# Kernel tuning notes

Hardware: AMD Instinct MI355X
Metric: run time of the kernel (lower is better)

## Reference

```python
import jax, jax.numpy as jnp
import numpy as np

R_MAX = 5.0          # MACE default cutoff
P_CUT = 6            # polynomial cutoff exponent
AVG_NEIGH = 16.0     # MACE avg_num_neighbors normalization


def _sph_harm(u):
    """Real spherical harmonics l=0..3, e3nn 'component' normalization. u: [E,3] unit vectors -> [E,16]."""
    x, y, z = u[..., 0], u[..., 1], u[..., 2]
    s3, s5, s15 = np.sqrt(3.0), np.sqrt(5.0), np.sqrt(15.0)
    s35_8, s105, s21_8, s7 = np.sqrt(35.0 / 8.0), np.sqrt(105.0), np.sqrt(21.0 / 8.0), np.sqrt(7.0)
    one = jnp.ones_like(x)
    Y = [
        one,
        s3 * x, s3 * y, s3 * z,
        s15 * x * y, s15 * y * z, 0.5 * s5 * (3.0 * z * z - 1.0), s15 * x * z, 0.5 * s15 * (x * x - y * y),
        s35_8 * y * (3.0 * x * x - y * y), s105 * x * y * z, s21_8 * y * (5.0 * z * z - 1.0),
        0.5 * s7 * (5.0 * z * z * z - 3.0 * z), s21_8 * x * (5.0 * z * z - 1.0),
        0.5 * s105 * z * (x * x - y * y), s35_8 * x * (x * x - 3.0 * y * y),
    ]
    return jnp.stack(Y, axis=-1)


def _radial_embedding(r):
    """Bessel basis (8) times polynomial cutoff. r: [E] -> [E,8]."""
    n = jnp.arange(1, 9, dtype=r.dtype)
    rb = np.sqrt(2.0 / R_MAX) * jnp.sin(n * jnp.pi * r[:, None] / R_MAX) / r[:, None]
    uu = jnp.clip(r / R_MAX, 0.0, 1.0)
    p = float(P_CUT)
    f = (1.0 - 0.5 * (p + 1.0) * (p + 2.0) * uu ** p
         + p * (p + 2.0) * uu ** (p + 1.0)
         - 0.5 * p * (p + 1.0) * uu ** (p + 2.0))
    return rb * f[:, None]


def _forward(positions, shifts, node_attrs, W_embed, W_up, W_r1, W_r2, W_lin, W_skip, W_prod, Wcg, Wcg2, edge_index):
    N = positions.shape[0]
    snd, rcv = edge_index[0], edge_index[1]
    vec = positions[rcv] - positions[snd] + shifts            # [E,3]
    r = jnp.sqrt(jnp.maximum(jnp.sum(vec * vec, -1), 1e-12))  # [E]
    u = vec / r[:, None]
    edge_attrs = _sph_harm(u)                                 # [E,16]
    edge_feats = _radial_embedding(r)                         # [E,8]
    L = edge_attrs.shape[-1]
    k = W_embed.shape[1]
    # node embedding: scalars in the l=0 slot
    feats = jnp.zeros((N, k, L), positions.dtype).at[:, :, 0].set(node_attrs @ W_embed)
    invariants = []
    for i in range(W_up.shape[0]):
        up = jnp.einsum('nkL,kc->ncL', feats, W_up[i])                      # linear_up
        Rw = jax.nn.silu(edge_feats @ W_r1[i]) @ W_r2[i]                    # radial MLP [E,k]
        gathered = up[snd] * Rw[:, :, None]                                 # [E,k,16]
        # equivariant tensor product (coupling tensor plays the CG role)
        msg = jnp.einsum('eka,es,ast->ekt', gathered, edge_attrs, Wcg)      # [E,k,16]
        agg = jax.ops.segment_sum(msg, rcv, num_segments=N) / AVG_NEIGH     # scatter-sum
        mid = jnp.einsum('nkL,kc->ncL', agg, W_lin[i])
        # residual skip tensor product with species attrs
        sc = jnp.einsum('nkL,nz,zkc->ncL', feats, node_attrs, W_skip[i])
        # product block: symmetric (quadratic) contraction + linear + skip
        quad = jnp.einsum('nka,nkb,abt->nkt', mid, mid, Wcg2)
        feats = jnp.einsum('nkL,kc->ncL', mid + quad, W_prod[i]) + sc
        invariants.append(feats[:, :, 0])                                   # l=0 invariant slice [N,k]
    return jnp.concatenate(invariants, axis=-1)                             # [N, n_layers*k]


def setup_inputs() -> dict:
    key = jax.random.key(0)
    ks = jax.random.split(key, 12)
    N, E, Z, k, L, NB, H, NL = 8000, 128000, 10, 32, 16, 8, 32, 2
    positions = jax.random.normal(ks[0], (N, 3), dtype=jnp.float32) * 2.0
    edge_index = jax.random.randint(ks[1], (2, E), 0, N, dtype=jnp.int32)
    shifts = jnp.zeros((E, 3), jnp.float32)
    species = jax.random.randint(ks[2], (N,), 0, Z)
    node_attrs = jax.nn.one_hot(species, Z, dtype=jnp.float32)
    W_embed = jax.random.normal(ks[3], (Z, k), dtype=jnp.float32) / np.sqrt(Z)
    W_up = jax.random.normal(ks[4], (NL, k, k), dtype=jnp.float32) / np.sqrt(k)
    W_r1 = jax.random.normal(ks[5], (NL, NB, H), dtype=jnp.float32) / np.sqrt(NB)
    W_r2 = jax.random.normal(ks[6], (NL, H, k), dtype=jnp.float32) / np.sqrt(H)
    W_lin = jax.random.normal(ks[7], (NL, k, k), dtype=jnp.float32) / np.sqrt(k)
    W_skip = jax.random.normal(ks[8], (NL, Z, k, k), dtype=jnp.float32) / np.sqrt(Z * k)
    W_prod = jax.random.normal(ks[9], (NL, k, k), dtype=jnp.float32) / np.sqrt(k)
    Wcg = jax.random.normal(ks[10], (L, L, L), dtype=jnp.float32) * 0.1
    Wcg2 = jax.random.normal(ks[11], (L, L, L), dtype=jnp.float32) * 0.05
    return dict(positions=positions, shifts=shifts, node_attrs=node_attrs, W_embed=W_embed,
                W_up=W_up, W_r1=W_r1, W_r2=W_r2, W_lin=W_lin, W_skip=W_skip, W_prod=W_prod,
                Wcg=Wcg, Wcg2=Wcg2, edge_index=edge_index)


def reference(positions, shifts, node_attrs, W_embed, W_up, W_r1, W_r2, W_lin, W_skip, W_prod, Wcg, Wcg2, edge_index):
    return _forward(positions, shifts, node_attrs, W_embed, W_up, W_r1, W_r2, W_lin, W_skip, W_prod, Wcg, Wcg2, edge_index)
```

## Files before the change

### kernel.cpp

```cpp
#include <hip/hip_runtime.h>
#include <math.h>
#include <stdint.h>

#define N_NODES 8000
#define N_EDGES 128000
#define NZ 10
#define K 32
#define LDIM 16
#define NB 8
#define NH 32
#define NL 2

typedef _Float16 half8 __attribute__((ext_vector_type(8)));
typedef _Float16 half2v __attribute__((ext_vector_type(2)));
typedef __attribute__((ext_vector_type(4))) float f32x4;

#define WAVE_SYNC() do { \
    asm volatile("s_waitcnt lgkmcnt(0)" ::: "memory"); \
    __builtin_amdgcn_wave_barrier(); \
    __builtin_amdgcn_sched_barrier(0); \
} while (0)

#define NBSTRIDE 640

__global__ __launch_bounds__(256) void k_count(const int* __restrict__ ei,
                                               int* __restrict__ counts) {
    int e = blockIdx.x * 256 + threadIdx.x;
    if (e >= N_EDGES) return;
    atomicAdd(&counts[ei[N_EDGES + e]], 1);
}

__global__ __launch_bounds__(1024) void k_scan(const int* __restrict__ counts,
                                               int* __restrict__ row_ptr,
                                               int* __restrict__ woff) {
    __shared__ int s[8192];
    int tid = threadIdx.x;
    for (int j = tid; j < 8192; j += 1024) s[j] = (j < N_NODES) ? counts[j] : 0;
    __syncthreads();
    for (int off = 1; off < 8192; off <<= 1) {
        int v[8];
#pragma unroll
        for (int jj = 0; jj < 8; jj++) {
            int idx = tid + jj*1024;
            v[jj] = s[idx] + ((idx >= off) ? s[idx - off] : 0);
        }
        __syncthreads();
#pragma unroll
        for (int jj = 0; jj < 8; jj++) s[tid + jj*1024] = v[jj];
        __syncthreads();
    }
    for (int j = tid; j <= N_NODES; j += 1024) {
        int v = (j == 0) ? 0 : s[j-1];
        row_ptr[j] = v;
        if (j < N_NODES) woff[j] = v;
    }
}

__global__ __launch_bounds__(256) void k_scatter(const int* __restrict__ ei,
                                                 int* __restrict__ woff,
                                                 int* __restrict__ inv,
                                                 int* __restrict__ snd_csr) {
    int e = blockIdx.x * 256 + threadIdx.x;
    if (e >= N_EDGES) return;
    int r = ei[N_EDGES + e];
    int s = ei[e];
    int pp = atomicAdd(&woff[r], 1);
    inv[e] = pp;
    snd_csr[pp] = s;
}

__global__ __launch_bounds__(256) void k_geom(const float* __restrict__ pos,
                                              const float* __restrict__ shifts,
                                              const int* __restrict__ ei,
                                              const int* __restrict__ inv,
                                              const float* __restrict__ Wcg,
                                              float* __restrict__ Yc,
                                              float* __restrict__ efc,
                                              float* __restrict__ C0c) {
    int e = blockIdx.x * blockDim.x + threadIdx.x;
    if (e >= N_EDGES) return;
    int snd = ei[e];
    int rcv = ei[N_EDGES + e];
    int slot = inv[e];
    float vx = pos[rcv*3+0] - pos[snd*3+0] + shifts[e*3+0];
    float vy = pos[rcv*3+1] - pos[snd*3+1] + shifts[e*3+1];
    float vz = pos[rcv*3+2] - pos[snd*3+2] + shifts[e*3+2];
    float r2 = vx*vx + vy*vy + vz*vz;
    float r  = sqrtf(fmaxf(r2, 1e-12f));
    float inv_r = 1.0f / r;
    float x = vx*inv_r, y = vy*inv_r, z = vz*inv_r;

    const float s3    = 1.7320508075688772f;
    const float s5    = 2.2360679774997896f;
    const float s15   = 3.8729833462074170f;
    const float s35_8 = 2.0916500663351885f;
    const float s105  = 10.246950765959598f;
    const float s21_8 = 1.6201851746019651f;
    const float s7    = 2.6457513110645907f;

    float Yv[16];
    Yv[0]  = 1.0f;
    Yv[1]  = s3*x;  Yv[2] = s3*y;  Yv[3] = s3*z;
    Yv[4]  = s15*x*y;
    Yv[5]  = s15*y*z;
    Yv[6]  = 0.5f*s5*(3.0f*z*z - 1.0f);
    Yv[7]  = s15*x*z;
    Yv[8]  = 0.5f*s15*(x*x - y*y);
    Yv[9]  = s35_8*y*(3.0f*x*x - y*y);
    Yv[10] = s105*x*y*z;
    Yv[11] = s21_8*y*(5.0f*z*z - 1.0f);
    Yv[12] = 0.5f*s7*(5.0f*z*z*z - 3.0f*z);
    Yv[13] = s21_8*x*(5.0f*z*z - 1.0f);
    Yv[14] = 0.5f*s105*z*(x*x - y*y);
    Yv[15] = s35_8*x*(x*x - 3.0f*y*y);
#pragma unroll
    for (int j = 0; j < 16; j++) Yc[(size_t)slot*16 + j] = Yv[j];

    {
        float c0[16];
#pragma unroll
        for (int t = 0; t < 16; ++t) c0[t] = 0.0f;
#pragma unroll
        for (int s = 0; s < 16; ++s) {
            const float4* w = (const float4*)(Wcg + s*16);
            float4 w0 = w[0], w1 = w[1], w2 = w[2], w3 = w[3];
            float ys = Yv[s];
            c0[0]+=ys*w0.x;  c0[1]+=ys*w0.y;  c0[2]+=ys*w0.z;  c0[3]+=ys*w0.w;
            c0[4]+=ys*w1.x;  c0[5]+=ys*w1.y;  c0[6]+=ys*w1.z;  c0[7]+=ys*w1.w;
            c0[8]+=ys*w2.x;  c0[9]+=ys*w2.y;  c0[10]+=ys*w2.z; c0[11]+=ys*w2.w;
            c0[12]+=ys*w3.x; c0[13]+=ys*w3.y; c0[14]+=ys*w3.z; c0[15]+=ys*w3.w;
        }
        float* o = C0c + (size_t)slot*16;
#pragma unroll
        for (int tq = 0; tq < 4; ++tq)
            *(float4*)(o + tq*4) = make_float4(c0[tq*4], c0[tq*4+1], c0[tq*4+2], c0[tq*4+3]);
    }

    float uu = fminf(fmaxf(r * 0.2f, 0.0f), 1.0f);
    float u2 = uu*uu;
    float u6 = u2*u2*u2;
    float f  = 1.0f - 28.0f*u6 + 48.0f*u6*uu - 21.0f*u6*u2;
    float c  = 0.632455532033676f * inv_r * f;
    const float PI5 = 3.14159265358979323846f * 0.2f;
#pragma unroll
    for (int n = 1; n <= 8; n++) efc[(size_t)slot*8 + n - 1] = c * sinf((float)n * PI5 * r);
}

__global__ __launch_bounds__(256) void k_ww(const float* __restrict__ We,
                                            const float* __restrict__ Wup0,
                                            float* __restrict__ WW) {
    int i = blockIdx.x * 256 + threadIdx.x;
    if (i >= NZ * K) return;
    int z = i >> 5, c = i & 31;
    float a = 0.0f;
#pragma unroll
    for (int k = 0; k < K; ++k) a += We[z*K + k] * Wup0[k*K + c];
    WW[i] = a;
}

__global__ __launch_bounds__(256) void k_wsym(const float* __restrict__ Wcg2,
                                              float* __restrict__ Wsym) {
    int j = blockIdx.x * 256 + threadIdx.x;
    if (j >= 136*16) return;
    int p = j >> 4, t = j & 15;
    int a = 0;
    for (int aa = 1; aa < 16; ++aa)
        if (p >= aa*16 - (aa*(aa-1))/2) a = aa;
    int b = a + (p - (a*16 - (a*(a-1))/2));
    float v = Wcg2[a*256 + b*16 + t];
    if (b > a) v += Wcg2[b*256 + a*16 + t];
    Wsym[j] = v;
}

__global__ __launch_bounds__(256) void k_embed(const float* __restrict__ attrs,
                                               const float* __restrict__ We,
                                               const float* __restrict__ WW,
                                               float* __restrict__ feats,
                                               float* __restrict__ up0c,
                                               int* __restrict__ spec) {
    int i = blockIdx.x * blockDim.x + threadIdx.x;
    if (i >= N_NODES * K) return;
    int n = i >> 5, k = i & 31;
    float a = 0.0f, b = 0.0f;
#pragma unroll
    for (int z = 0; z < NZ; z++) {
        float av = attrs[n*NZ + z];
        a += av * We[z*K + k];
        b += av * WW[z*K + k];
    }
    float* f = feats + (size_t)n*(K*LDIM) + k*LDIM;
    f[0] = a;
#pragma unroll
    for (int j = 1; j < LDIM; j++) f[j] = 0.0f;
    up0c[(size_t)n*K + k] = b;
    if (k == 0) {
        int sp = 0; float best = -1.0f;
        for (int z = 0; z < NZ; z++) { float v = attrs[n*NZ + z]; if (v > best) { best = v; sp = z; } }
        spec[n] = sp;
    }
}

__global__ __launch_bounds__(256) void k_radial(const float* __restrict__ efc,
                                                const float* __restrict__ W1,
                                                const float* __restrict__ W2,
                                                float* __restrict__ Rwc) {
    __shared__ __align__(16) float lW1[NB*NH];
    __shared__ __align__(16) float lW2[NH*K];
    int tid = threadIdx.x;
    for (int j = tid; j < NB*NH; j += 256) lW1[j] = W1[j];
    for (int j = tid; j < NH*K;  j += 256) lW2[j] = W2[j];
    __syncthreads();
    int e = blockIdx.x * 256 + tid;
    if (e >= N_EDGES) return;
    const float4* e4 = (const float4*)(efc + (size_t)e*8);
    float4 ea = e4[0], eb = e4[1];
    float efr[8] = {ea.x, ea.y, ea.z, ea.w, eb.x, eb.y, eb.z, eb.w};
    float rw[32];
#pragma unroll
    for (int k = 0; k < 32; ++k) rw[k] = 0.0f;
    for (int j = 0; j < NH; ++j) {
        float h = 0.0f;
#pragma unroll
        for (int b = 0; b < NB; ++b) h += efr[b] * lW1[b*NH + j];
        float s = h / (1.0f + expf(-h));
        const float4* w2r = (const float4*)(lW2 + j*K);
#pragma unroll
        for (int kq = 0; kq < 8; ++kq) {
            float4 w = w2r[kq];
            rw[kq*4+0] += s*w.x; rw[kq*4+1] += s*w.y;
            rw[kq*4+2] += s*w.z; rw[kq*4+3] += s*w.w;
        }
    }
    float4* o = (float4*)(Rwc + (size_t)e*32);
#pragma unroll
    for (int kq = 0; kq < 8; ++kq)
        o[kq] = make_float4(rw[kq*4], rw[kq*4+1], rw[kq*4+2], rw[kq*4+3]);
}

__device__ __forceinline__ void node_update(float* nb,
                                            const float* lWlin, const float* lWprod,
                                            const float* lWup, const float* lWsym,
                                            const float* __restrict__ Wskip,
                                            float* __restrict__ feats,
                                            const int* __restrict__ spec,
                                            float* __restrict__ out,
                                            int n, int lane, int layer,
                                            _Float16* __restrict__ up_next, int has_up) {
    int c  = lane & 31;
    int th = lane >> 5;
    int to = th * 8;

    float m8[8] = {0,0,0,0,0,0,0,0};
#pragma clang loop unroll_count(4)
    for (int k = 0; k < 32; ++k) {
        float w = lWlin[k*32 + c];
        float4 a0 = *(const float4*)(nb + k*20 + to);
        float4 a1 = *(const float4*)(nb + k*20 + to + 4);
        m8[0]+=a0.x*w; m8[1]+=a0.y*w; m8[2]+=a0.z*w; m8[3]+=a0.w*w;
        m8[4]+=a1.x*w; m8[5]+=a1.y*w; m8[6]+=a1.z*w; m8[7]+=a1.w*w;
    }
    WAVE_SYNC();
    *(float4*)(nb + c*20 + to)     = make_float4(m8[0],m8[1],m8[2],m8[3]);
    *(float4*)(nb + c*20 + to + 4) = make_float4(m8[4],m8[5],m8[6],m8[7]);
    WAVE_SYNC();
    float m[16];
#pragma unroll
    for (int j = 0; j < 4; ++j) {
        float4 v = *(const float4*)(nb + c*20 + j*4);
        m[j*4]=v.x; m[j*4+1]=v.y; m[j*4+2]=v.z; m[j*4+3]=v.w;
    }

    float q8[8] = {0,0,0,0,0,0,0,0};
    {
        int p = 0;
#pragma clang loop unroll(disable)
        for (int a = 0; a < 16; ++a) {
            float ma = m[a];
#pragma clang loop unroll_count(2)
            for (int b = a; b < 16; ++b) {
                float pm = ma * m[b];
                float4 w0 = *(const float4*)(lWsym + p*16 + to);
                float4 w1 = *(const float4*)(lWsym + p*16 + to + 4);
                q8[0]+=pm*w0.x; q8[1]+=pm*w0.y; q8[2]+=pm*w0.z; q8[3]+=pm*w0.w;
                q8[4]+=pm*w1.x; q8[5]+=pm*w1.y; q8[6]+=pm*w1.z; q8[7]+=pm*w1.w;
                ++p;
            }
        }
    }

    WAVE_SYNC();
    *(float4*)(nb + c*20 + to)     = make_float4(m[to]+q8[0],   m[to+1]+q8[1],
                                                 m[to+2]+q8[2], m[to+3]+q8[3]);
    *(float4*)(nb + c*20 + to + 4) = make_float4(m[to+4]+q8[4], m[to+5]+q8[5],
                                                 m[to+6]+q8[6], m[to+7]+q8[7]);
    WAVE_SYNC();

    int sp = spec[n];
    const float* wsk = Wskip + (size_t)sp*1024;
    float* fg = feats + (size_t)n*512;
    float acc8[8] = {0,0,0,0,0,0,0,0};
#pragma clang loop unroll_count(4)
    for (int k = 0; k < 32; ++k) {
        float wp = lWprod[k*32 + c];
        float wv = wsk[k*32 + c];
        float4 s0 = *(const float4*)(nb + k*20 + to);
        float4 s1 = *(const float4*)(nb + k*20 + to + 4);
        float4 f0 = *(const float4*)(fg + k*16 + to);
        float4 f1 = *(const float4*)(fg + k*16 + to + 4);
        acc8[0]+=s0.x*wp+f0.x*wv; acc8[1]+=s0.y*wp+f0.y*wv;
        acc8[2]+=s0.z*wp+f0.z*wv; acc8[3]+=s0.w*wp+f0.w*wv;
        acc8[4]+=s1.x*wp+f1.x*wv; acc8[5]+=s1.y*wp+f1.y*wv;
        acc8[6]+=s1.z*wp+f1.z*wv; acc8[7]+=s1.w*wp+f1.w*wv;
    }
    if (th == 0) out[(size_t)n*(NL*K) + layer*K + c] = acc8[0];
    *(float4*)(fg + c*16 + to)     = make_float4(acc8[0],acc8[1],acc8[2],acc8[3]);
    *(float4*)(fg + c*16 + to + 4) = make_float4(acc8[4],acc8[5],acc8[6],acc8[7]);

    if (has_up) {
        WAVE_SYNC();
        *(float4*)(nb + c*20 + to)     = make_float4(acc8[0],acc8[1],acc8[2],acc8[3]);
        *(float4*)(nb + c*20 + to + 4) = make_float4(acc8[4],acc8[5],acc8[6],acc8[7]);
        WAVE_SYNC();
        float u8[8] = {0,0,0,0,0,0,0,0};
#pragma clang loop unroll_count(4)
        for (int k = 0; k < 32; ++k) {
            float w = lWup[k*32 + c];
            float4 f0 = *(const float4*)(nb + k*20 + to);
            float4 f1 = *(const float4*)(nb + k*20 + to + 4);
            u8[0]+=f0.x*w; u8[1]+=f0.y*w; u8[2]+=f0.z*w; u8[3]+=f0.w*w;
            u8[4]+=f1.x*w; u8[5]+=f1.y*w; u8[6]+=f1.z*w; u8[7]+=f1.w*w;
        }
        half8 h;
#pragma unroll
        for (int j = 0; j < 8; ++j) h[j] = (_Float16)u8[j];
        *(half8*)(up_next + (size_t)n*512 + c*16 + to) = h;
    }
}

__global__ __launch_bounds__(256, 4) void k_fused0(const float* __restrict__ up0c,
                                                   const float* __restrict__ C0c,
                                                   const float* __restrict__ Rwc,
                                                   const int* __restrict__ snd_csr,
                                                   const int* __restrict__ row_ptr,
                                                   const float* __restrict__ Wlin,
                                                   const float* __restrict__ Wskip,
                                                   const float* __restrict__ Wprod,
                                                   const float* __restrict__ WsymG,
                                                   const float* __restrict__ Wup_next,
                                                   float* __restrict__ feats,
                                                   const int* __restrict__ spec,
                                                   float* __restrict__ out,
                                                   _Float16* __restrict__ up_next) {
    __shared__ __align__(16) float lWlin[1024];
    __shared__ __align__(16) float lWprod[1024];
    __shared__ __align__(16) float lWup[1024];
    __shared__ __align__(16) float lWsym[2176];
    __shared__ __align__(16) float buf[4*NBSTRIDE];

    int tid = threadIdx.x;
    for (int j = tid; j < 1024; j += 256) { lWlin[j] = Wlin[j]; lWprod[j] = Wprod[j]; lWup[j] = Wup_next[j]; }
    for (int j = tid; j < 2176; j += 256) lWsym[j] = WsymG[j];
    __syncthreads();

    int wave = tid >> 6, lane = tid & 63;
    int n = blockIdx.x * 4 + wave;
    int k0 = lane & 15, tq = lane >> 4;
    float* nb = buf + wave*NBSTRIDE;

    int start = row_ptr[n], end = row_ptr[n+1];
    float4 acc0 = {0,0,0,0}, acc1 = {0,0,0,0};

    if (start < end) {
        int snd = snd_csr[start];
        float4 c0v = *(const float4*)(C0c + (size_t)start*16 + tq*4);
        float rw0 = Rwc[(size_t)start*32 + k0];
        float rw1 = Rwc[(size_t)start*32 + 16 + k0];
        float u0 = up0c[(size_t)snd*32 + k0];
        float u1 = up0c[(size_t)snd*32 + 16 + k0];

        for (int ii = start; ii < end; ++ii) {
            int ip = (ii + 1 < end) ? ii + 1 : ii;
            int nsnd = snd_csr[ip];
            float4 nc0v = *(const float4*)(C0c + (size_t)ip*16 + tq*4);
            float nrw0 = Rwc[(size_t)ip*32 + k0];
            float nrw1 = Rwc[(size_t)ip*32 + 16 + k0];
            float nu0 = up0c[(size_t)nsnd*32 + k0];
            float nu1 = up0c[(size_t)nsnd*32 + 16 + k0];

            float g0 = rw0 * u0, g1 = rw1 * u1;
            acc0.x += g0*c0v.x; acc0.y += g0*c0v.y; acc0.z += g0*c0v.z; acc0.w += g0*c0v.w;
            acc1.x += g1*c0v.x; acc1.y += g1*c0v.y; acc1.z += g1*c0v.z; acc1.w += g1*c0v.w;

            c0v = nc0v; rw0 = nrw0; rw1 = nrw1; u0 = nu0; u1 = nu1;
        }
    }

    *(float4*)(nb + k0*20 + tq*4)      = make_float4(acc0.x*0.0625f, acc0.y*0.0625f,
                                                     acc0.z*0.0625f, acc0.w*0.0625f);
    *(float4*)(nb + (16+k0)*20 + tq*4) = make_float4(acc1.x*0.0625f, acc1.y*0.0625f,
                                                     acc1.z*0.0625f, acc1.w*0.0625f);
    WAVE_SYNC();

    node_update(nb, lWlin, lWprod, lWup, lWsym, Wskip, feats, spec, out, n, lane, 0, up_next, 1);
}

__global__ __launch_bounds__(256, 3) void k_fused1(const _Float16* __restrict__ up,
                                                   const float* __restrict__ Yc,
                                                   const float* __restrict__ Rwc,
                                                   const int* __restrict__ snd_csr,
                                                   const int* __restrict__ row_ptr,
                                                   const float* __restrict__ Wcg,
                                                   const float* __restrict__ Wlin,
                                                   const float* __restrict__ Wskip,
                                                   const float* __restrict__ Wprod,
                                                   const float* __restrict__ WsymG,
                                                   float* __restrict__ feats,
                                                   const int* __restrict__ spec,
                                                   float* __restrict__ out) {
    __shared__ __align__(16) float lWlin[1024];
    __shared__ __align__(16) float lWprod[1024];
    __shared__ __align__(16) float lWsym[2176];
    __shared__ __align__(16) float buf[4*NBSTRIDE];

    int tid = threadIdx.x;
    for (int j = tid; j < 1024; j += 256) { lWlin[j] = Wlin[j]; lWprod[j] = Wprod[j]; }
    for (int j = tid; j < 2176; j += 256) lWsym[j] = WsymG[j];
    __syncthreads();

    int wave = tid >> 6, lane = tid & 63;
    int n = blockIdx.x * 4 + wave;
    int t0 = lane & 15;
    int g  = lane >> 4;
    int h  = g & 1;
    int eo = g >> 1;
    float* nb = buf + wave*NBSTRIDE;

    half2v wrh[16][4];
#pragma unroll
    for (int s = 0; s < 16; ++s)
#pragma unroll
        for (int q = 0; q < 4; ++q) {
            half2v w;
            w[0] = (_Float16)Wcg[(8*h + 2*q    )*256 + s*16 + t0];
            w[1] = (_Float16)Wcg[(8*h + 2*q + 1)*256 + s*16 + t0];
            wrh[s][q] = w;
        }

    int start = row_ptr[n], end = row_ptr[n+1];
    f32x4 accL = {0.f,0.f,0.f,0.f}, accH = {0.f,0.f,0.f,0.f};

    if (start < end) {
        int i0 = start + eo;     bool v0 = i0 < end; int q0 = v0 ? i0 : start;
        int i1 = i0 + 2;         bool v1 = i1 < end; int q1 = v1 ? i1 : start;
        int i2 = i0 + 4;         bool v2 = i2 < end; int q2 = v2 ? i2 : start;
        int snd0 = snd_csr[q0], snd1 = snd_csr[q1];
        int snd2 = snd_csr[q2];

        const float4* Y4 = (const float4*)(Yc + (size_t)q0*16);
        float4 y0=Y4[0], y1=Y4[1], y2=Y4[2], y3=Y4[3];
        float rwL = v0 ? Rwc[(size_t)q0*32 + t0]      : 0.0f;
        float rwH = v0 ? Rwc[(size_t)q0*32 + 16 + t0] : 0.0f;
        half8 u0L = *(const half8*)(up + (size_t)snd0*512 + t0*16 + 8*h);
        half8 u0H = *(const half8*)(up + (size_t)snd0*512 + (16+t0)*16 + 8*h);
        half8 u1L = *(const half8*)(up + (size_t)snd1*512 + t0*16 + 8*h);
        half8 u1H = *(const half8*)(up + (size_t)snd1*512 + (16+t0)*16 + 8*h);

        int npair = (end - start + 1) >> 1;
        for (int p = 0; p < npair; ++p) {
            half8 u2L = *(const half8*)(up + (size_t)snd2*512 + t0*16 + 8*h);
            half8 u2H = *(const half8*)(up + (size_t)snd2*512 + (16+t0)*16 + 8*h);
            int in1 = start + 2*(p+1) + eo; bool vn1 = in1 < end; int qn1 = vn1 ? in1 : start;
            const float4* nY = (const float4*)(Yc + (size_t)qn1*16);
            float4 ny0=nY[0], ny1=nY[1], ny2=nY[2], ny3=nY[3];
            float nrwL = vn1 ? Rwc[(size_t)qn1*32 + t0]      : 0.0f;
            float nrwH = vn1 ? Rwc[(size_t)qn1*32 + 16 + t0] : 0.0f;
            int in3 = start + 2*(p+3) + eo; bool vn3 = in3 < end; int qn3 = vn3 ? in3 : start;
            int snd3 = snd_csr[qn3];

            float yv[16] = {y0.x,y0.y,y0.z,y0.w, y1.x,y1.y,y1.z,y1.w,
                            y2.x,y2.y,y2.z,y2.w, y3.x,y3.y,y3.z,y3.w};
            half2v ch[4];
#pragma unroll
            for (int q = 0; q < 4; ++q) { half2v z; z[0]=(_Float16)0.f; z[1]=(_Float16)0.f; ch[q]=z; }
#pragma unroll
            for (int s = 0; s < 16; ++s) {
                _Float16 yh = (_Float16)yv[s];
                half2v yb; yb[0] = yh; yb[1] = yh;
#pragma unroll
                for (int q = 0; q < 4; ++q) ch[q] += yb * wrh[s][q];
            }
            half8 bf;
#pragma unroll
            for (int q = 0; q < 4; ++q) { bf[2*q] = ch[q][0]; bf[2*q+1] = ch[q][1]; }

            half8 rvL, rvH;
            _Float16 rwLh = (_Float16)rwL, rwHh = (_Float16)rwH;
#pragma unroll
            for (int j = 0; j < 8; ++j) { rvL[j] = rwLh; rvH[j] = rwHh; }
            half8 afL = u0L * rvL;
            half8 afH = u0H * rvH;

            accL = __builtin_amdgcn_mfma_f32_16x16x32_f16(afL, bf, accL, 0, 0, 0);
            accH = __builtin_amdgcn_mfma_f32_16x16x32_f16(afH, bf, accH, 0, 0, 0);

            y0=ny0; y1=ny1; y2=ny2; y3=ny3;
            rwL=nrwL; rwH=nrwH;
            u0L=u1L; u0H=u1H; u1L=u2L; u1H=u2H;
            snd2 = snd3;
        }
    }

#pragma unroll
    for (int e = 0; e < 4; ++e) {
        nb[(4*g + e)*20 + t0]      = accL[e] * 0.0625f;
        nb[(16 + 4*g + e)*20 + t0] = accH[e] * 0.0625f;
    }
    WAVE_SYNC();

    node_update(nb, lWlin, lWprod, (const float*)nullptr, lWsym, Wskip, feats, spec, out,
                n, lane, 1, (_Float16*)nullptr, 0);
}

extern "C" void kernel_launch(void* const* d_in, const int* in_sizes, int n_in,
                              void* d_out, int out_size, void* d_ws, size_t ws_size,
                              hipStream_t stream) {
    const float* pos     = (const float*)d_in[0];
    const float* shifts  = (const float*)d_in[1];
    const float* attrs   = (const float*)d_in[2];
    const float* W_embed = (const float*)d_in[3];
    const float* W_up    = (const float*)d_in[4];
    const float* W_r1    = (const float*)d_in[5];
    const float* W_r2    = (const float*)d_in[6];
    const float* W_lin   = (const float*)d_in[7];
    const float* W_skip  = (const float*)d_in[8];
    const float* W_prod  = (const float*)d_in[9];
    const float* Wcg     = (const float*)d_in[10];
    const float* Wcg2    = (const float*)d_in[11];
    const int*   ei      = (const int*)d_in[12];
    float* out = (float*)d_out;

    uint8_t* p = (uint8_t*)d_ws;
    auto alloc = [&](size_t bytes) -> void* {
        void* r = (void*)p;
        p += (bytes + 255) & ~size_t(255);
        return r;
    };
    float* Yc        = (float*)alloc((size_t)N_EDGES * 16 * sizeof(float));
    float* efc       = (float*)alloc((size_t)N_EDGES * 8  * sizeof(float));
    float* C0c       = (float*)alloc((size_t)N_EDGES * 16 * sizeof(float));
    float* Rwc0      = (float*)alloc((size_t)N_EDGES * K  * sizeof(float));
    float* Rwc1      = (float*)alloc((size_t)N_EDGES * K  * sizeof(float));
    float* feats     = (float*)alloc((size_t)N_NODES * K * LDIM * sizeof(float));
    _Float16* up_h   = (_Float16*)alloc((size_t)N_NODES * K * LDIM * sizeof(_Float16));
    float* up0c      = (float*)alloc((size_t)N_NODES * K * sizeof(float));
    float* WW        = (float*)alloc((size_t)NZ * K * sizeof(float));
    float* Wsym      = (float*)alloc((size_t)136 * 16 * sizeof(float));
    int* counts   = (int*)alloc((size_t)N_NODES * sizeof(int));
    int* woff     = (int*)alloc((size_t)N_NODES * sizeof(int));
    int* row_ptr  = (int*)alloc((size_t)(N_NODES + 1) * sizeof(int));
    int* inv      = (int*)alloc((size_t)N_EDGES * sizeof(int));
    int* snd_csr  = (int*)alloc((size_t)N_EDGES * sizeof(int));
    int* spec     = (int*)alloc((size_t)N_NODES * sizeof(int));

    hipMemsetAsync(counts, 0, N_NODES * sizeof(int), stream);
    k_count<<<(N_EDGES + 255) / 256, 256, 0, stream>>>(ei, counts);
    k_scan<<<1, 1024, 0, stream>>>(counts, row_ptr, woff);
    k_scatter<<<(N_EDGES + 255) / 256, 256, 0, stream>>>(ei, woff, inv, snd_csr);
    k_geom<<<(N_EDGES + 255) / 256, 256, 0, stream>>>(pos, shifts, ei, inv, Wcg, Yc, efc, C0c);
    k_ww<<<2, 256, 0, stream>>>(W_embed, W_up, WW);
    k_wsym<<<(136*16 + 255) / 256, 256, 0, stream>>>(Wcg2, Wsym);
    k_embed<<<(N_NODES * K + 255) / 256, 256, 0, stream>>>(attrs, W_embed, WW, feats, up0c, spec);

    k_radial<<<(N_EDGES + 255) / 256, 256, 0, stream>>>(efc, W_r1, W_r2, Rwc0);
    k_radial<<<(N_EDGES + 255) / 256, 256, 0, stream>>>(efc, W_r1 + (size_t)1*NB*NH,
                                                        W_r2 + (size_t)1*NH*K, Rwc1);

    k_fused0<<<N_NODES/4, 256, 0, stream>>>(up0c, C0c, Rwc0, snd_csr, row_ptr,
                                            W_lin, W_skip, W_prod, Wsym,
                                            W_up + (size_t)1*K*K,
                                            feats, spec, out, up_h);

    k_fused1<<<N_NODES/4, 256, 0, stream>>>(up_h, Yc, Rwc1, snd_csr, row_ptr, Wcg,
                                            W_lin + (size_t)1*K*K,
                                            W_skip + (size_t)1*NZ*K*K,
                                            W_prod + (size_t)1*K*K, Wsym,
                                            feats, spec, out);
}
```

Before: 246.2 us.

## Precompute per-edge CG matrices in fp16 and stream them into fused layer-1 kernel

Adds a separate kernel that computes each edge's 16x16 contraction of Wcg with the spherical harmonics and stores it in fp16 (a transposed Wcg copy is built first). The layer-1 fused kernel then loads that precomputed B operand for the MFMA instead of rebuilding it per edge from Yc and register-held Wcg. The per-edge FMA work and the 64 register-resident weight pairs go away, and the occupancy hint is raised from 3 to 4 waves. In exchange it writes and reads a 64 MB intermediate (512 bytes per edge) through HBM, adds a kernel launch, and the fp16 rounding point moves.

```diff
diff --git a/kernel.cpp b/kernel.cpp
--- a/kernel.cpp
+++ b/kernel.cpp
@@ -12,7 +12,6 @@
 #define NL 2
 
 typedef _Float16 half8 __attribute__((ext_vector_type(8)));
-typedef _Float16 half2v __attribute__((ext_vector_type(2)));
 typedef __attribute__((ext_vector_type(4))) float f32x4;
 
 #define WAVE_SYNC() do { \
@@ -146,6 +145,46 @@
     for (int n = 1; n <= 8; n++) efc[(size_t)slot*8 + n - 1] = c * sinf((float)n * PI5 * r);
 }
 
+__global__ __launch_bounds__(256) void k_wt(const float* __restrict__ Wcg,
+                                            float* __restrict__ WcgT) {
+    int j = blockIdx.x * 256 + threadIdx.x;
+    if (j >= 4096) return;
+    int a = j >> 8, s = (j >> 4) & 15, t = j & 15;
+    WcgT[t*256 + s*16 + a] = Wcg[j];
+}
+
+__global__ __launch_bounds__(256) void k_cbuild(const float* __restrict__ Yc,
+                                                const float* __restrict__ WcgT,
+                                                _Float16* __restrict__ C1c) {
+    int i = blockIdx.x * 256 + threadIdx.x;
+    if (i >= N_EDGES * 16) return;
+    int slot = i >> 4, t = i & 15;
+    const float4* Y4 = (const float4*)(Yc + (size_t)slot*16);
+    float4 ya = Y4[0], yb = Y4[1], yc = Y4[2], yd = Y4[3];
+    float yv[16] = {ya.x,ya.y,ya.z,ya.w, yb.x,yb.y,yb.z,yb.w,
+                    yc.x,yc.y,yc.z,yc.w, yd.x,yd.y,yd.z,yd.w};
+    const float* wt = WcgT + t*256;
+    float c[16];
+#pragma unroll
+    for (int a = 0; a < 16; ++a) c[a] = 0.0f;
+#pragma unroll
+    for (int s = 0; s < 16; ++s) {
+        const float4* w = (const float4*)(wt + s*16);
+        float4 w0 = w[0], w1 = w[1], w2 = w[2], w3 = w[3];
+        float ys = yv[s];
+        c[0]+=ys*w0.x;  c[1]+=ys*w0.y;  c[2]+=ys*w0.z;  c[3]+=ys*w0.w;
+        c[4]+=ys*w1.x;  c[5]+=ys*w1.y;  c[6]+=ys*w1.z;  c[7]+=ys*w1.w;
+        c[8]+=ys*w2.x;  c[9]+=ys*w2.y;  c[10]+=ys*w2.z; c[11]+=ys*w2.w;
+        c[12]+=ys*w3.x; c[13]+=ys*w3.y; c[14]+=ys*w3.z; c[15]+=ys*w3.w;
+    }
+    half8 h0, h1;
+#pragma unroll
+    for (int j = 0; j < 8; ++j) { h0[j] = (_Float16)c[j]; h1[j] = (_Float16)c[8+j]; }
+    _Float16* o = C1c + (size_t)slot*256 + t*16;
+    *(half8*)(o)     = h0;
+    *(half8*)(o + 8) = h1;
+}
+
 __global__ __launch_bounds__(256) void k_ww(const float* __restrict__ We,
                                             const float* __restrict__ Wup0,
                                             float* __restrict__ WW) {
@@ -404,12 +443,11 @@
     node_update(nb, lWlin, lWprod, lWup, lWsym, Wskip, feats, spec, out, n, lane, 0, up_next, 1);
 }
 
-__global__ __launch_bounds__(256, 3) void k_fused1(const _Float16* __restrict__ up,
-                                                   const float* __restrict__ Yc,
+__global__ __launch_bounds__(256, 4) void k_fused1(const _Float16* __restrict__ up,
+                                                   const _Float16* __restrict__ C1c,
                                                    const float* __restrict__ Rwc,
                                                    const int* __restrict__ snd_csr,
                                                    const int* __restrict__ row_ptr,
-                                                   const float* __restrict__ Wcg,
                                                    const float* __restrict__ Wlin,
                                                    const float* __restrict__ Wskip,
                                                    const float* __restrict__ Wprod,
@@ -435,17 +473,6 @@
     int eo = g >> 1;
     float* nb = buf + wave*NBSTRIDE;
 
-    half2v wrh[16][4];
-#pragma unroll
-    for (int s = 0; s < 16; ++s)
-#pragma unroll
-        for (int q = 0; q < 4; ++q) {
-            half2v w;
-            w[0] = (_Float16)Wcg[(8*h + 2*q    )*256 + s*16 + t0];
-            w[1] = (_Float16)Wcg[(8*h + 2*q + 1)*256 + s*16 + t0];
-            wrh[s][q] = w;
-        }
-
     int start = row_ptr[n], end = row_ptr[n+1];
     f32x4 accL = {0.f,0.f,0.f,0.f}, accH = {0.f,0.f,0.f,0.f};
 
@@ -456,8 +483,7 @@
         int snd0 = snd_csr[q0], snd1 = snd_csr[q1];
         int snd2 = snd_csr[q2];
 
-        const float4* Y4 = (const float4*)(Yc + (size_t)q0*16);
-        float4 y0=Y4[0], y1=Y4[1], y2=Y4[2], y3=Y4[3];
+        half8 bf0 = *(const half8*)(C1c + (size_t)q0*256 + t0*16 + 8*h);
         float rwL = v0 ? Rwc[(size_t)q0*32 + t0]      : 0.0f;
         float rwH = v0 ? Rwc[(size_t)q0*32 + 16 + t0] : 0.0f;
         half8 u0L = *(const half8*)(up + (size_t)snd0*512 + t0*16 + 8*h);
@@ -470,29 +496,12 @@
             half8 u2L = *(const half8*)(up + (size_t)snd2*512 + t0*16 + 8*h);
             half8 u2H = *(const half8*)(up + (size_t)snd2*512 + (16+t0)*16 + 8*h);
             int in1 = start + 2*(p+1) + eo; bool vn1 = in1 < end; int qn1 = vn1 ? in1 : start;
-            const float4* nY = (const float4*)(Yc + (size_t)qn1*16);
-            float4 ny0=nY[0], ny1=nY[1], ny2=nY[2], ny3=nY[3];
+            half8 nbf = *(const half8*)(C1c + (size_t)qn1*256 + t0*16 + 8*h);
             float nrwL = vn1 ? Rwc[(size_t)qn1*32 + t0]      : 0.0f;
             float nrwH = vn1 ? Rwc[(size_t)qn1*32 + 16 + t0] : 0.0f;
             int in3 = start + 2*(p+3) + eo; bool vn3 = in3 < end; int qn3 = vn3 ? in3 : start;
             int snd3 = snd_csr[qn3];
 
-            float yv[16] = {y0.x,y0.y,y0.z,y0.w, y1.x,y1.y,y1.z,y1.w,
-                            y2.x,y2.y,y2.z,y2.w, y3.x,y3.y,y3.z,y3.w};
-            half2v ch[4];
-#pragma unroll
-            for (int q = 0; q < 4; ++q) { half2v z; z[0]=(_Float16)0.f; z[1]=(_Float16)0.f; ch[q]=z; }
-#pragma unroll
-            for (int s = 0; s < 16; ++s) {
-                _Float16 yh = (_Float16)yv[s];
-                half2v yb; yb[0] = yh; yb[1] = yh;
-#pragma unroll
-                for (int q = 0; q < 4; ++q) ch[q] += yb * wrh[s][q];
-            }
-            half8 bf;
-#pragma unroll
-            for (int q = 0; q < 4; ++q) { bf[2*q] = ch[q][0]; bf[2*q+1] = ch[q][1]; }
-
             half8 rvL, rvH;
             _Float16 rwLh = (_Float16)rwL, rwHh = (_Float16)rwH;
 #pragma unroll
@@ -500,12 +509,12 @@
             half8 afL = u0L * rvL;
             half8 afH = u0H * rvH;
 
-            accL = __builtin_amdgcn_mfma_f32_16x16x32_f16(afL, bf, accL, 0, 0, 0);
-            accH = __builtin_amdgcn_mfma_f32_16x16x32_f16(afH, bf, accH, 0, 0, 0);
-
-            y0=ny0; y1=ny1; y2=ny2; y3=ny3;
-            rwL=nrwL; rwH=nrwH;
-            u0L=u1L; u0H=u1H; u1L=u2L; u1H=u2H;
+            accL = __builtin_amdgcn_mfma_f32_16x16x32_f16(afL, bf0, accL, 0, 0, 0);
+            accH = __builtin_amdgcn_mfma_f32_16x16x32_f16(afH, bf0, accH, 0, 0, 0);
+
+            bf0 = nbf;
+            rwL = nrwL; rwH = nrwH;
+            u0L = u1L; u0H = u1H; u1L = u2L; u1H = u2H;
             snd2 = snd3;
         }
     }
@@ -548,6 +557,7 @@
     float* Yc        = (float*)alloc((size_t)N_EDGES * 16 * sizeof(float));
     float* efc       = (float*)alloc((size_t)N_EDGES * 8  * sizeof(float));
     float* C0c       = (float*)alloc((size_t)N_EDGES * 16 * sizeof(float));
+    _Float16* C1c    = (_Float16*)alloc((size_t)N_EDGES * 256 * sizeof(_Float16));
     float* Rwc0      = (float*)alloc((size_t)N_EDGES * K  * sizeof(float));
     float* Rwc1      = (float*)alloc((size_t)N_EDGES * K  * sizeof(float));
     float* feats     = (float*)alloc((size_t)N_NODES * K * LDIM * sizeof(float));
@@ -555,6 +565,7 @@
     float* up0c      = (float*)alloc((size_t)N_NODES * K * sizeof(float));
     float* WW        = (float*)alloc((size_t)NZ * K * sizeof(float));
     float* Wsym      = (float*)alloc((size_t)136 * 16 * sizeof(float));
+    float* WcgT      = (float*)alloc((size_t)4096 * sizeof(float));
     int* counts   = (int*)alloc((size_t)N_NODES * sizeof(int));
     int* woff     = (int*)alloc((size_t)N_NODES * sizeof(int));
     int* row_ptr  = (int*)alloc((size_t)(N_NODES + 1) * sizeof(int));
@@ -567,6 +578,8 @@
     k_scan<<<1, 1024, 0, stream>>>(counts, row_ptr, woff);
     k_scatter<<<(N_EDGES + 255) / 256, 256, 0, stream>>>(ei, woff, inv, snd_csr);
     k_geom<<<(N_EDGES + 255) / 256, 256, 0, stream>>>(pos, shifts, ei, inv, Wcg, Yc, efc, C0c);
+    k_wt<<<16, 256, 0, stream>>>(Wcg, WcgT);
+    k_cbuild<<<(N_EDGES * 16 + 255) / 256, 256, 0, stream>>>(Yc, WcgT, C1c);
     k_ww<<<2, 256, 0, stream>>>(W_embed, W_up, WW);
     k_wsym<<<(136*16 + 255) / 256, 256, 0, stream>>>(Wcg2, Wsym);
     k_embed<<<(N_NODES * K + 255) / 256, 256, 0, stream>>>(attrs, W_embed, WW, feats, up0c, spec);
@@ -580,7 +593,7 @@
                                             W_up + (size_t)1*K*K,
                                             feats, spec, out, up_h);
 
-    k_fused1<<<N_NODES/4, 256, 0, stream>>>(up_h, Yc, Rwc1, snd_csr, row_ptr, Wcg,
+    k_fused1<<<N_NODES/4, 256, 0, stream>>>(up_h, C1c, Rwc1, snd_csr, row_ptr,
                                             W_lin + (size_t)1*K*K,
                                             W_skip + (size_t)1*NZ*K*K,
                                             W_prod + (size_t)1*K*K, Wsym,
```

After: 465.7 us. 89.2% more time.

## Split each node across two waves in fused message and node-update kernels

Applied to the files above, without the earlier changes.

Each node is now handled by two wavefronts (128 threads) instead of one. The edges are interleaved between the two waves, their partial sums are combined through shared memory, and the node update works on 4 L-components per thread instead of 8. The aim is to double parallelism per node, shorten the serial edge loop and the per-thread register load, and raise k_fused1 occupancy. The cost is twice as many blocks, each reloading the weights into shared memory, plus block-wide __syncthreads in place of wave-local syncs.

```diff
diff --git a/kernel.cpp b/kernel.cpp
--- a/kernel.cpp
+++ b/kernel.cpp
@@ -12,14 +12,9 @@
 #define NL 2
 
 typedef _Float16 half8 __attribute__((ext_vector_type(8)));
+typedef _Float16 half4v __attribute__((ext_vector_type(4)));
 typedef _Float16 half2v __attribute__((ext_vector_type(2)));
 typedef __attribute__((ext_vector_type(4))) float f32x4;
-
-#define WAVE_SYNC() do { \
-    asm volatile("s_waitcnt lgkmcnt(0)" ::: "memory"); \
-    __builtin_amdgcn_wave_barrier(); \
-    __builtin_amdgcn_sched_barrier(0); \
-} while (0)
 
 #define NBSTRIDE 640
 
@@ -237,32 +232,27 @@
         o[kq] = make_float4(rw[kq*4], rw[kq*4+1], rw[kq*4+2], rw[kq*4+3]);
 }
 
-__device__ __forceinline__ void node_update(float* nb,
-                                            const float* lWlin, const float* lWprod,
-                                            const float* lWup, const float* lWsym,
-                                            const float* __restrict__ Wskip,
-                                            float* __restrict__ feats,
-                                            const int* __restrict__ spec,
-                                            float* __restrict__ out,
-                                            int n, int lane, int layer,
-                                            _Float16* __restrict__ up_next, int has_up) {
-    int c  = lane & 31;
-    int th = lane >> 5;
-    int to = th * 8;
-
-    float m8[8] = {0,0,0,0,0,0,0,0};
+__device__ __forceinline__ void node_update128(float* nb,
+                                               const float* lWlin, const float* lWprod,
+                                               const float* lWup, const float* lWsym,
+                                               const float* __restrict__ Wskip,
+                                               float* __restrict__ feats,
+                                               const int* __restrict__ spec,
+                                               float* __restrict__ out,
+                                               int n, int c, int th, int layer,
+                                               _Float16* __restrict__ up_next, int has_up) {
+    int to = th * 4;
+
+    float m4[4] = {0,0,0,0};
 #pragma clang loop unroll_count(4)
     for (int k = 0; k < 32; ++k) {
         float w = lWlin[k*32 + c];
         float4 a0 = *(const float4*)(nb + k*20 + to);
-        float4 a1 = *(const float4*)(nb + k*20 + to + 4);
-        m8[0]+=a0.x*w; m8[1]+=a0.y*w; m8[2]+=a0.z*w; m8[3]+=a0.w*w;
-        m8[4]+=a1.x*w; m8[5]+=a1.y*w; m8[6]+=a1.z*w; m8[7]+=a1.w*w;
-    }
-    WAVE_SYNC();
-    *(float4*)(nb + c*20 + to)     = make_float4(m8[0],m8[1],m8[2],m8[3]);
-    *(float4*)(nb + c*20 + to + 4) = make_float4(m8[4],m8[5],m8[6],m8[7]);
-    WAVE_SYNC();
+        m4[0]+=a0.x*w; m4[1]+=a0.y*w; m4[2]+=a0.z*w; m4[3]+=a0.w*w;
+    }
+    __syncthreads();
+    *(float4*)(nb + c*20 + to) = make_float4(m4[0],m4[1],m4[2],m4[3]);
+    __syncthreads();
     float m[16];
 #pragma unroll
     for (int j = 0; j < 4; ++j) {
@@ -270,70 +260,58 @@
         m[j*4]=v.x; m[j*4+1]=v.y; m[j*4+2]=v.z; m[j*4+3]=v.w;
     }
 
-    float q8[8] = {0,0,0,0,0,0,0,0};
+    float q4[4] = {0,0,0,0};
     {
         int p = 0;
 #pragma clang loop unroll(disable)
         for (int a = 0; a < 16; ++a) {
             float ma = m[a];
-#pragma clang loop unroll_count(2)
+#pragma clang loop unroll_count(4)
             for (int b = a; b < 16; ++b) {
                 float pm = ma * m[b];
                 float4 w0 = *(const float4*)(lWsym + p*16 + to);
-                float4 w1 = *(const float4*)(lWsym + p*16 + to + 4);
-                q8[0]+=pm*w0.x; q8[1]+=pm*w0.y; q8[2]+=pm*w0.z; q8[3]+=pm*w0.w;
-                q8[4]+=pm*w1.x; q8[5]+=pm*w1.y; q8[6]+=pm*w1.z; q8[7]+=pm*w1.w;
+                q4[0]+=pm*w0.x; q4[1]+=pm*w0.y; q4[2]+=pm*w0.z; q4[3]+=pm*w0.w;
                 ++p;
             }
         }
     }
 
-    WAVE_SYNC();
-    *(float4*)(nb + c*20 + to)     = make_float4(m[to]+q8[0],   m[to+1]+q8[1],
-                                                 m[to+2]+q8[2], m[to+3]+q8[3]);
-    *(float4*)(nb + c*20 + to + 4) = make_float4(m[to+4]+q8[4], m[to+5]+q8[5],
-                                                 m[to+6]+q8[6], m[to+7]+q8[7]);
-    WAVE_SYNC();
+    __syncthreads();
+    *(float4*)(nb + c*20 + to) = make_float4(m[to]+q4[0], m[to+1]+q4[1],
+                                             m[to+2]+q4[2], m[to+3]+q4[3]);
+    __syncthreads();
 
     int sp = spec[n];
     const float* wsk = Wskip + (size_t)sp*1024;
     float* fg = feats + (size_t)n*512;
-    float acc8[8] = {0,0,0,0,0,0,0,0};
+    float acc4[4] = {0,0,0,0};
 #pragma clang loop unroll_count(4)
     for (int k = 0; k < 32; ++k) {
         float wp = lWprod[k*32 + c];
         float wv = wsk[k*32 + c];
         float4 s0 = *(const float4*)(nb + k*20 + to);
-        float4 s1 = *(const float4*)(nb + k*20 + to + 4);
         float4 f0 = *(const float4*)(fg + k*16 + to);
-        float4 f1 = *(const float4*)(fg + k*16 + to + 4);
-        acc8[0]+=s0.x*wp+f0.x*wv; acc8[1]+=s0.y*wp+f0.y*wv;
-        acc8[2]+=s0.z*wp+f0.z*wv; acc8[3]+=s0.w*wp+f0.w*wv;
-        acc8[4]+=s1.x*wp+f1.x*wv; acc8[5]+=s1.y*wp+f1.y*wv;
-        acc8[6]+=s1.z*wp+f1.z*wv; acc8[7]+=s1.w*wp+f1.w*wv;
-    }
-    if (th == 0) out[(size_t)n*(NL*K) + layer*K + c] = acc8[0];
-    *(float4*)(fg + c*16 + to)     = make_float4(acc8[0],acc8[1],acc8[2],acc8[3]);
-    *(float4*)(fg + c*16 + to + 4) = make_float4(acc8[4],acc8[5],acc8[6],acc8[7]);
+        acc4[0]+=s0.x*wp+f0.x*wv; acc4[1]+=s0.y*wp+f0.y*wv;
+        acc4[2]+=s0.z*wp+f0.z*wv; acc4[3]+=s0.w*wp+f0.w*wv;
+    }
+    if (th == 0) out[(size_t)n*(NL*K) + layer*K + c] = acc4[0];
+    *(float4*)(fg + c*16 + to) = make_float4(acc4[0],acc4[1],acc4[2],acc4[3]);
 
     if (has_up) {
-        WAVE_SYNC();
-        *(float4*)(nb + c*20 + to)     = make_float4(acc8[0],acc8[1],acc8[2],acc8[3]);
-        *(float4*)(nb + c*20 + to + 4) = make_float4(acc8[4],acc8[5],acc8[6],acc8[7]);
-        WAVE_SYNC();
-        float u8[8] = {0,0,0,0,0,0,0,0};
+        __syncthreads();
+        *(float4*)(nb + c*20 + to) = make_float4(acc4[0],acc4[1],acc4[2],acc4[3]);
+        __syncthreads();
+        float u4[4] = {0,0,0,0};
 #pragma clang loop unroll_count(4)
         for (int k = 0; k < 32; ++k) {
             float w = lWup[k*32 + c];
             float4 f0 = *(const float4*)(nb + k*20 + to);
-            float4 f1 = *(const float4*)(nb + k*20 + to + 4);
-            u8[0]+=f0.x*w; u8[1]+=f0.y*w; u8[2]+=f0.z*w; u8[3]+=f0.w*w;
-            u8[4]+=f1.x*w; u8[5]+=f1.y*w; u8[6]+=f1.z*w; u8[7]+=f1.w*w;
-        }
-        half8 h;
-#pragma unroll
-        for (int j = 0; j < 8; ++j) h[j] = (_Float16)u8[j];
-        *(half8*)(up_next + (size_t)n*512 + c*16 + to) = h;
+            u4[0]+=f0.x*w; u4[1]+=f0.y*w; u4[2]+=f0.z*w; u4[3]+=f0.w*w;
+        }
+        half4v h;
+#pragma unroll
+        for (int j = 0; j < 4; ++j) h[j] = (_Float16)u4[j];
+        *(half4v*)(up_next + (size_t)n*512 + c*16 + to) = h;
     }
 }
 
@@ -355,7 +333,7 @@
     __shared__ __align__(16) float lWprod[1024];
     __shared__ __align__(16) float lWup[1024];
     __shared__ __align__(16) float lWsym[2176];
-    __shared__ __align__(16) float buf[4*NBSTRIDE];
+    __shared__ __align__(16) float buf[2*NBSTRIDE];
 
     int tid = threadIdx.x;
     for (int j = tid; j < 1024; j += 256) { lWlin[j] = Wlin[j]; lWprod[j] = Wprod[j]; lWup[j] = Wup_next[j]; }
@@ -363,23 +341,25 @@
     __syncthreads();
 
     int wave = tid >> 6, lane = tid & 63;
-    int n = blockIdx.x * 4 + wave;
+    int nd = wave >> 1, sub = wave & 1;
+    int n = blockIdx.x * 2 + nd;
     int k0 = lane & 15, tq = lane >> 4;
-    float* nb = buf + wave*NBSTRIDE;
+    float* nb = buf + nd*NBSTRIDE;
 
     int start = row_ptr[n], end = row_ptr[n+1];
     float4 acc0 = {0,0,0,0}, acc1 = {0,0,0,0};
 
-    if (start < end) {
-        int snd = snd_csr[start];
-        float4 c0v = *(const float4*)(C0c + (size_t)start*16 + tq*4);
-        float rw0 = Rwc[(size_t)start*32 + k0];
-        float rw1 = Rwc[(size_t)start*32 + 16 + k0];
+    if (start + sub < end) {
+        int ii0 = start + sub;
+        int snd = snd_csr[ii0];
+        float4 c0v = *(const float4*)(C0c + (size_t)ii0*16 + tq*4);
+        float rw0 = Rwc[(size_t)ii0*32 + k0];
+        float rw1 = Rwc[(size_t)ii0*32 + 16 + k0];
         float u0 = up0c[(size_t)snd*32 + k0];
         float u1 = up0c[(size_t)snd*32 + 16 + k0];
 
-        for (int ii = start; ii < end; ++ii) {
-            int ip = (ii + 1 < end) ? ii + 1 : ii;
+        for (int ii = ii0; ii < end; ii += 2) {
+            int ip = (ii + 2 < end) ? ii + 2 : ii;
             int nsnd = snd_csr[ip];
             float4 nc0v = *(const float4*)(C0c + (size_t)ip*16 + tq*4);
             float nrw0 = Rwc[(size_t)ip*32 + k0];
@@ -395,16 +375,28 @@
         }
     }
 
-    *(float4*)(nb + k0*20 + tq*4)      = make_float4(acc0.x*0.0625f, acc0.y*0.0625f,
-                                                     acc0.z*0.0625f, acc0.w*0.0625f);
-    *(float4*)(nb + (16+k0)*20 + tq*4) = make_float4(acc1.x*0.0625f, acc1.y*0.0625f,
-                                                     acc1.z*0.0625f, acc1.w*0.0625f);
-    WAVE_SYNC();
-
-    node_update(nb, lWlin, lWprod, lWup, lWsym, Wskip, feats, spec, out, n, lane, 0, up_next, 1);
-}
-
-__global__ __launch_bounds__(256, 3) void k_fused1(const _Float16* __restrict__ up,
+    const float sc = 0.0625f;
+    if (sub == 0) {
+        *(float4*)(nb + k0*20 + tq*4)      = make_float4(acc0.x*sc, acc0.y*sc, acc0.z*sc, acc0.w*sc);
+        *(float4*)(nb + (16+k0)*20 + tq*4) = make_float4(acc1.x*sc, acc1.y*sc, acc1.z*sc, acc1.w*sc);
+    }
+    __syncthreads();
+    if (sub == 1) {
+        float4 o0 = *(const float4*)(nb + k0*20 + tq*4);
+        float4 o1 = *(const float4*)(nb + (16+k0)*20 + tq*4);
+        *(float4*)(nb + k0*20 + tq*4)      = make_float4(o0.x+acc0.x*sc, o0.y+acc0.y*sc,
+                                                         o0.z+acc0.z*sc, o0.w+acc0.w*sc);
+        *(float4*)(nb + (16+k0)*20 + tq*4) = make_float4(o1.x+acc1.x*sc, o1.y+acc1.y*sc,
+                                                         o1.z+acc1.z*sc, o1.w+acc1.w*sc);
+    }
+    __syncthreads();
+
+    int c = lane & 31;
+    int th = (sub << 1) | (lane >> 5);
+    node_update128(nb, lWlin, lWprod, lWup, lWsym, Wskip, feats, spec, out, n, c, th, 0, up_next, 1);
+}
+
+__global__ __launch_bounds__(256, 4) void k_fused1(const _Float16* __restrict__ up,
                                                    const float* __restrict__ Yc,
                                                    const float* __restrict__ Rwc,
                                                    const int* __restrict__ snd_csr,
@@ -420,7 +412,7 @@
     __shared__ __align__(16) float lWlin[1024];
     __shared__ __align__(16) float lWprod[1024];
     __shared__ __align__(16) float lWsym[2176];
-    __shared__ __align__(16) float buf[4*NBSTRIDE];
+    __shared__ __align__(16) float buf[2*NBSTRIDE];
 
     int tid = threadIdx.x;
     for (int j = tid; j < 1024; j += 256) { lWlin[j] = Wlin[j]; lWprod[j] = Wprod[j]; }
@@ -428,12 +420,13 @@
     __syncthreads();
 
     int wave = tid >> 6, lane = tid & 63;
-    int n = blockIdx.x * 4 + wave;
+    int nd = wave >> 1, sub = wave & 1;
+    int n = blockIdx.x * 2 + nd;
     int t0 = lane & 15;
     int g  = lane >> 4;
     int h  = g & 1;
     int eo = g >> 1;
-    float* nb = buf + wave*NBSTRIDE;
+    float* nb = buf + nd*NBSTRIDE;
 
     half2v wrh[16][4];
 #pragma unroll
@@ -448,11 +441,12 @@
 
     int start = row_ptr[n], end = row_ptr[n+1];
     f32x4 accL = {0.f,0.f,0.f,0.f}, accH = {0.f,0.f,0.f,0.f};
-
-    if (start < end) {
-        int i0 = start + eo;     bool v0 = i0 < end; int q0 = v0 ? i0 : start;
-        int i1 = i0 + 2;         bool v1 = i1 < end; int q1 = v1 ? i1 : start;
-        int i2 = i0 + 4;         bool v2 = i2 < end; int q2 = v2 ? i2 : start;
+    int np = (end - start + 1) >> 1;
+
+    if (sub < np) {
+        int i0 = start + 2*sub + eo;         bool v0 = i0 < end; int q0 = v0 ? i0 : start;
+        int i1 = start + 2*(sub+2) + eo;     bool v1 = i1 < end; int q1 = v1 ? i1 : start;
+        int i2 = start + 2*(sub+4) + eo;     bool v2 = i2 < end; int q2 = v2 ? i2 : start;
         int snd0 = snd_csr[q0], snd1 = snd_csr[q1];
         int snd2 = snd_csr[q2];
 
@@ -465,16 +459,15 @@
         half8 u1L = *(const half8*)(up + (size_t)snd1*512 + t0*16 + 8*h);
         half8 u1H = *(const half8*)(up + (size_t)snd1*512 + (16+t0)*16 + 8*h);
 
-        int npair = (end - start + 1) >> 1;
-        for (int p = 0; p < npair; ++p) {
+        for (int p = sub; p < np; p += 2) {
             half8 u2L = *(const half8*)(up + (size_t)snd2*512 + t0*16 + 8*h);
             half8 u2H = *(const half8*)(up + (size_t)snd2*512 + (16+t0)*16 + 8*h);
-            int in1 = start + 2*(p+1) + eo; bool vn1 = in1 < end; int qn1 = vn1 ? in1 : start;
+            int in1 = start + 2*(p+2) + eo; bool vn1 = in1 < end; int qn1 = vn1 ? in1 : start;
             const float4* nY = (const float4*)(Yc + (size_t)qn1*16);
             float4 ny0=nY[0], ny1=nY[1], ny2=nY[2], ny3=nY[3];
             float nrwL = vn1 ? Rwc[(size_t)qn1*32 + t0]      : 0.0f;
             float nrwH = vn1 ? Rwc[(size_t)qn1*32 + 16 + t0] : 0.0f;
-            int in3 = start + 2*(p+3) + eo; bool vn3 = in3 < end; int qn3 = vn3 ? in3 : start;
+            int in3 = start + 2*(p+6) + eo; bool vn3 = in3 < end; int qn3 = vn3 ? in3 : start;
             int snd3 = snd_csr[qn3];
 
             float yv[16] = {y0.x,y0.y,y0.z,y0.w, y1.x,y1.y,y1.z,y1.w,
@@ -510,15 +503,28 @@
         }
     }
 
-#pragma unroll
-    for (int e = 0; e < 4; ++e) {
-        nb[(4*g + e)*20 + t0]      = accL[e] * 0.0625f;
-        nb[(16 + 4*g + e)*20 + t0] = accH[e] * 0.0625f;
-    }
-    WAVE_SYNC();
-
-    node_update(nb, lWlin, lWprod, (const float*)nullptr, lWsym, Wskip, feats, spec, out,
-                n, lane, 1, (_Float16*)nullptr, 0);
+    const float sc = 0.0625f;
+    if (sub == 0) {
+#pragma unroll
+        for (int e = 0; e < 4; ++e) {
+            nb[(4*g + e)*20 + t0]      = accL[e] * sc;
+            nb[(16 + 4*g + e)*20 + t0] = accH[e] * sc;
+        }
+    }
+    __syncthreads();
+    if (sub == 1) {
+#pragma unroll
+        for (int e = 0; e < 4; ++e) {
+            nb[(4*g + e)*20 + t0]      += accL[e] * sc;
+            nb[(16 + 4*g + e)*20 + t0] += accH[e] * sc;
+        }
+    }
+    __syncthreads();
+
+    int c = lane & 31;
+    int th = (sub << 1) | (lane >> 5);
+    node_update128(nb, lWlin, lWprod, (const float*)nullptr, lWsym, Wskip, feats, spec, out,
+                   n, c, th, 1, (_Float16*)nullptr, 0);
 }
 
 extern "C" void kernel_launch(void* const* d_in, const int* in_sizes, int n_in,
@@ -575,12 +581,12 @@
     k_radial<<<(N_EDGES + 255) / 256, 256, 0, stream>>>(efc, W_r1 + (size_t)1*NB*NH,
                                                         W_r2 + (size_t)1*NH*K, Rwc1);
 
-    k_fused0<<<N_NODES/4, 256, 0, stream>>>(up0c, C0c, Rwc0, snd_csr, row_ptr,
+    k_fused0<<<N_NODES/2, 256, 0, stream>>>(up0c, C0c, Rwc0, snd_csr, row_ptr,
                                             W_lin, W_skip, W_prod, Wsym,
                                             W_up + (size_t)1*K*K,
                                             feats, spec, out, up_h);
 
-    k_fused1<<<N_NODES/4, 256, 0, stream>>>(up_h, Yc, Rwc1, snd_csr, row_ptr, Wcg,
+    k_fused1<<<N_NODES/2, 256, 0, stream>>>(up_h, Yc, Rwc1, snd_csr, row_ptr, Wcg,
                                             W_lin + (size_t)1*K*K,
                                             W_skip + (size_t)1*NZ*K*K,
                                             W_prod + (size_t)1*K*K, Wsym,
```

After: 415.0 us. +68.6%, slower.
